# Kernel optimization log

Measured on AMD Instinct MI355X. Metric: run time of the kernel, lower is better.

The kernel has to match this reference:

```python
import jax, jax.numpy as jnp
import numpy as np

IN_DIM = 512
E = 512            # embed_dim
DI = 1024          # d_inner = expand * embed_dim
S = 16             # d_state
DC = 4             # d_conv
DT_RANK = 32       # ceil(embed_dim / 16)
NL = 2             # n_layers
N_SLICES = 8000
CHUNK = 500        # hard-coded batch_size in forward


def setup_inputs() -> dict:
    key = jax.random.key(0)
    ks = jax.random.split(key, 16)
    s = 0.02
    inp = {
        "slice_features": jax.random.normal(ks[0], (N_SLICES, IN_DIM), dtype=jnp.float32),
        "ip_w": jax.random.normal(ks[1], (E, IN_DIM), dtype=jnp.float32) * s,
        "ip_b": jnp.zeros((E,), jnp.float32),
        "in_ln_g": jnp.ones((E,), jnp.float32),
        "in_ln_b": jnp.zeros((E,), jnp.float32),
        "m_in_w": jax.random.normal(ks[2], (NL, 2 * DI, E), dtype=jnp.float32) * s,
        "m_conv_w": jax.random.normal(ks[3], (NL, DI, DC), dtype=jnp.float32) * s,
        "m_conv_b": jnp.zeros((NL, DI), jnp.float32),
        "m_xproj_w": jax.random.normal(ks[4], (NL, DT_RANK + 2 * S, DI), dtype=jnp.float32) * s,
        "m_dt_w": jax.random.normal(ks[5], (NL, DI, DT_RANK), dtype=jnp.float32) * s,
        "m_dt_b": jax.random.normal(ks[6], (NL, DI), dtype=jnp.float32) * 0.1,
        "m_Alog": jnp.log(jnp.tile(jnp.arange(1, S + 1, dtype=jnp.float32), (NL, DI, 1))),
        "m_D": jnp.ones((NL, DI), jnp.float32),
        "m_out_w": jax.random.normal(ks[7], (NL, E, DI), dtype=jnp.float32) * s,
        "ln_g": jnp.ones((NL, E), jnp.float32),
        "ln_b": jnp.zeros((NL, E), jnp.float32),
        "op_w": jax.random.normal(ks[8], (E, E), dtype=jnp.float32) * s,
        "op_b": jnp.zeros((E,), jnp.float32),
    }
    return inp


def _layer_norm(x, g, b):
    mu = jnp.mean(x, axis=-1, keepdims=True)
    var = jnp.mean(jnp.square(x - mu), axis=-1, keepdims=True)
    return (x - mu) * jax.lax.rsqrt(var + 1e-5) * g + b


def _mamba(h, in_w, conv_w, conv_b, xproj_w, dt_w, dt_b, Alog, Dp, out_w):
    # h: (Nc, L, E) -> (Nc, L, E)
    Nc, L, _ = h.shape
    xz = jnp.einsum('nle,de->nld', h, in_w)          # (Nc, L, 2*DI)
    x, z = jnp.split(xz, 2, axis=-1)
    # causal depthwise conv1d along L
    k = jnp.transpose(conv_w)[:, None, :]            # (DC, 1, DI) WIO grouped
    x = jax.lax.conv_general_dilated(
        x, k, window_strides=(1,), padding=[(DC - 1, 0)],
        dimension_numbers=('NWC', 'WIO', 'NWC'), feature_group_count=DI) + conv_b
    x = jax.nn.silu(x)
    x_dbl = jnp.einsum('nld,rd->nlr', x, xproj_w)    # (Nc, L, DT_RANK + 2S)
    dt = jax.nn.softplus(jnp.einsum('nlr,dr->nld', x_dbl[..., :DT_RANK], dt_w) + dt_b)
    B = x_dbl[..., DT_RANK:DT_RANK + S]
    C = x_dbl[..., DT_RANK + S:]
    A = -jnp.exp(Alog)                               # (DI, S)

    def step(hs, inp):
        dt_t, B_t, C_t, x_t = inp                    # (Nc,DI),(Nc,S),(Nc,S),(Nc,DI)
        dA = jnp.exp(dt_t[..., None] * A)            # (Nc, DI, S)
        hs = dA * hs + (dt_t * x_t)[..., None] * B_t[:, None, :]
        y = jnp.einsum('nds,ns->nd', hs, C_t)
        return hs, y

    xs = (jnp.swapaxes(dt, 0, 1), jnp.swapaxes(B, 0, 1),
          jnp.swapaxes(C, 0, 1), jnp.swapaxes(x, 0, 1))
    h0 = jnp.zeros((Nc, DI, S), dt.dtype)
    _, ys = jax.lax.scan(step, h0, xs)               # ys: (L, Nc, DI)
    y = jnp.swapaxes(ys, 0, 1) + x * Dp
    y = y * jax.nn.silu(z)
    return jnp.einsum('nld,ed->nle', y, out_w)


def reference(slice_features, ip_w, ip_b, in_ln_g, in_ln_b, m_in_w, m_conv_w, m_conv_b,
              m_xproj_w, m_dt_w, m_dt_b, m_Alog, m_D, m_out_w, ln_g, ln_b, op_w, op_b):
    h = slice_features @ ip_w.T + ip_b               # (N, E)
    h = _layer_norm(h, in_ln_g, in_ln_b)             # dropout: eval no-op
    h = h.reshape(N_SLICES // CHUNK, CHUNK, E)       # chunks of 500, batched
    for l in range(NL):
        res = h
        h = _mamba(h, m_in_w[l], m_conv_w[l], m_conv_b[l], m_xproj_w[l],
                   m_dt_w[l], m_dt_b[l], m_Alog[l], m_D[l], m_out_w[l])
        h = _layer_norm(h + res, ln_g[l], ln_b[l])
    h = h.reshape(N_SLICES, E)
    return h @ op_w.T + op_b
```

## Files before the change

kernel.cpp:

```cpp
#include <hip/hip_runtime.h>
#include <hip/hip_bf16.h>
#include <math.h>

#define NSL 8000
#define MPAD 8064
#define EDIM 512
#define DI_ 1024
#define SDIM 16
#define NLAY 2
#define CHK 500
#define PSEG 10
#define LSEG 50

typedef __bf16 bf16_t;
typedef bf16_t bf16x8 __attribute__((ext_vector_type(8)));
typedef bf16_t bf16x4 __attribute__((ext_vector_type(4)));
typedef float  f32x4  __attribute__((ext_vector_type(4)));

#define GL2LDS(g, l) __builtin_amdgcn_global_load_lds( \
    (const __attribute__((address_space(1))) void*)(g), \
    (__attribute__((address_space(3))) void*)(l), 16, 0, 0)

template<int EPI>
__global__ __launch_bounds__(256)
void gemm_mfma(const bf16_t* __restrict__ Ah, const bf16_t* __restrict__ Al,
               const bf16_t* __restrict__ Wh, const bf16_t* __restrict__ Wl,
               const float* __restrict__ bias, float* __restrict__ C,
               float* __restrict__ C2, int M, int N, int K)
{
    __shared__ bf16_t sm[4 * 128 * 64];
    const int tid = threadIdx.x;
    const int w   = tid >> 6;
    const int l   = tid & 63;
    const int m0  = blockIdx.y * 128;
    const int n0  = blockIdx.x * 128;

    const bf16_t* gb0 = Ah + (size_t)m0 * K;
    const bf16_t* gb1 = Al + (size_t)m0 * K;
    const bf16_t* gb2 = Wh + (size_t)n0 * K;
    const bf16_t* gb3 = Wl + (size_t)n0 * K;

    const int srow = l >> 3;
    const int scol = ((l & 7) ^ (l >> 3)) * 8;

    const int wm = (w >> 1) * 64;
    const int wn = (w & 1) * 64;
    const int lr = l & 15;
    const int lk = (l >> 4) * 8;
    const int csw = (l & 7) << 3;

    f32x4 acc[4][4];
    #pragma unroll
    for (int i = 0; i < 4; ++i)
        #pragma unroll
        for (int j = 0; j < 4; ++j) acc[i][j] = (f32x4){0.f,0.f,0.f,0.f};

    for (int kt = 0; kt < K; kt += 64) {
        #pragma unroll
        for (int i = 0; i < 16; ++i) {
            const int mat = i >> 2;
            const int lc  = ((i & 3) << 2) | w;
            const bf16_t* gsrc;
            if      (mat == 0) gsrc = gb0;
            else if (mat == 1) gsrc = gb1;
            else if (mat == 2) gsrc = gb2;
            else               gsrc = gb3;
            const bf16_t* gp = gsrc + (size_t)(lc * 8 + srow) * K + kt + scol;
            bf16_t* lp = sm + mat * 8192 + lc * 512;
            GL2LDS(gp, lp);
        }
        __syncthreads();
        #pragma unroll
        for (int ks = 0; ks < 2; ++ks) {
            bf16x8 ah[4], al[4], wh[4], wl[4];
            const int koff = (ks * 32 + lk) ^ csw;
            #pragma unroll
            for (int f = 0; f < 4; ++f) {
                const int ar = wm + f * 16 + lr;
                const int wr = wn + f * 16 + lr;
                ah[f] = *(const bf16x8*)(sm + 0 * 8192 + ar * 64 + koff);
                al[f] = *(const bf16x8*)(sm + 1 * 8192 + ar * 64 + koff);
                wh[f] = *(const bf16x8*)(sm + 2 * 8192 + wr * 64 + koff);
                wl[f] = *(const bf16x8*)(sm + 3 * 8192 + wr * 64 + koff);
            }
            #pragma unroll
            for (int fi = 0; fi < 4; ++fi)
                #pragma unroll
                for (int fj = 0; fj < 4; ++fj) {
                    acc[fi][fj] = __builtin_amdgcn_mfma_f32_16x16x32_bf16(ah[fi], wh[fj], acc[fi][fj], 0, 0, 0);
                    acc[fi][fj] = __builtin_amdgcn_mfma_f32_16x16x32_bf16(ah[fi], wl[fj], acc[fi][fj], 0, 0, 0);
                    acc[fi][fj] = __builtin_amdgcn_mfma_f32_16x16x32_bf16(al[fi], wh[fj], acc[fi][fj], 0, 0, 0);
                }
        }
        __syncthreads();
    }
    const int r4 = (l >> 4) * 4;
    #pragma unroll
    for (int fj = 0; fj < 4; ++fj) {
        const int col = n0 + wn + fj * 16 + lr;
        if (EPI == 3 && col >= 1056) continue;
        const float bv = (EPI == 1) ? bias[col]
                       : (EPI == 3 ? (col < 1024 ? bias[col] : 0.f) : 0.f);
        #pragma unroll
        for (int fi = 0; fi < 4; ++fi) {
            const int rowb = m0 + wm + fi * 16 + r4;
            #pragma unroll
            for (int r = 0; r < 4; ++r) {
                const int row = rowb + r;
                if (row >= M) continue;
                float v = acc[fi][fj][r] + bv;
                if (EPI == 3) {
                    if (col < 1024) {
                        v = fmaxf(v, 0.f) + log1pf(__expf(-fabsf(v)));
                        C[(size_t)row * 1024 + col] = v;
                    } else {
                        C2[(size_t)row * 32 + (col - 1024)] = v;
                    }
                } else {
                    C[(size_t)row * N + col] = v;
                }
            }
        }
    }
}

__global__ __launch_bounds__(256)
void compose_dtw(const float* __restrict__ dtw,
                 const float* __restrict__ xp,
                 bf16_t* __restrict__ wh, bf16_t* __restrict__ wl)
{
    const int d0 = blockIdx.x * 4;
    const int t  = threadIdx.x;
    float acc[4][4] = {{0.f}};
    for (int r = 0; r < 32; ++r) {
        float xv[4];
        #pragma unroll
        for (int cc = 0; cc < 4; ++cc) xv[cc] = xp[r * 1024 + t + cc * 256];
        #pragma unroll
        for (int dd = 0; dd < 4; ++dd) {
            float wv = dtw[(d0 + dd) * 32 + r];
            #pragma unroll
            for (int cc = 0; cc < 4; ++cc) acc[dd][cc] = fmaf(wv, xv[cc], acc[dd][cc]);
        }
    }
    #pragma unroll
    for (int dd = 0; dd < 4; ++dd)
        #pragma unroll
        for (int cc = 0; cc < 4; ++cc) {
            float v = acc[dd][cc];
            bf16_t hb = (bf16_t)v;
            size_t o = (size_t)(d0 + dd) * 1024 + t + cc * 256;
            wh[o] = hb;
            wl[o] = (bf16_t)(v - (float)hb);
        }
}

__global__ __launch_bounds__(256)
void ln_kernel(const float* __restrict__ in, const float* __restrict__ res,
               const float* __restrict__ g, const float* __restrict__ b,
               float* __restrict__ out, bf16_t* __restrict__ oh, bf16_t* __restrict__ ol)
{
    const int lane = threadIdx.x & 63;
    const int wv = threadIdx.x >> 6;
    const int row = blockIdx.x * 4 + wv;
    const size_t base = (size_t)row * EDIM + lane * 8;
    float x[8];
    float4 v0 = *(const float4*)(in + base);
    float4 v1 = *(const float4*)(in + base + 4);
    x[0]=v0.x; x[1]=v0.y; x[2]=v0.z; x[3]=v0.w;
    x[4]=v1.x; x[5]=v1.y; x[6]=v1.z; x[7]=v1.w;
    if (res) {
        float4 r0 = *(const float4*)(res + base);
        float4 r1 = *(const float4*)(res + base + 4);
        x[0]+=r0.x; x[1]+=r0.y; x[2]+=r0.z; x[3]+=r0.w;
        x[4]+=r1.x; x[5]+=r1.y; x[6]+=r1.z; x[7]+=r1.w;
    }
    float s = 0.f, sq = 0.f;
    #pragma unroll
    for (int j = 0; j < 8; ++j) { s += x[j]; sq += x[j]*x[j]; }
    #pragma unroll
    for (int off = 32; off; off >>= 1) {
        s  += __shfl_xor(s, off);
        sq += __shfl_xor(sq, off);
    }
    float mu = s * (1.f/EDIM);
    float var = sq * (1.f/EDIM) - mu*mu;
    float rs = rsqrtf(var + 1e-5f);
    const int col = lane * 8;
    float o[8];
    bf16x8 vh, vl;
    #pragma unroll
    for (int j = 0; j < 8; ++j) {
        o[j] = (x[j] - mu) * rs * g[col+j] + b[col+j];
        bf16_t hb = (bf16_t)o[j];
        vh[j] = hb;
        vl[j] = (bf16_t)(o[j] - (float)hb);
    }
    *(float4*)(out + base)     = make_float4(o[0],o[1],o[2],o[3]);
    *(float4*)(out + base + 4) = make_float4(o[4],o[5],o[6],o[7]);
    *(bf16x8*)(oh + base) = vh;
    *(bf16x8*)(ol + base) = vl;
}

__global__ __launch_bounds__(256)
void conv_silu_k(const float* __restrict__ xz, const float* __restrict__ w,
                 const float* __restrict__ b, bf16_t* __restrict__ xch,
                 bf16_t* __restrict__ xcl)
{
    const int d  = blockIdx.x * 256 + threadIdx.x;
    const int lc = blockIdx.y;
    const int n  = blockIdx.z;
    const int l0 = lc * 100;
    const float w0 = w[d*4+0], w1 = w[d*4+1], w2 = w[d*4+2], w3 = w[d*4+3];
    const float bb = b[d];
    const float* xp = xz + (size_t)n * CHK * 2048 + d;
    float x0 = (l0-3) >= 0 ? xp[(size_t)(l0-3)*2048] : 0.f;
    float x1 = (l0-2) >= 0 ? xp[(size_t)(l0-2)*2048] : 0.f;
    float x2 = (l0-1) >= 0 ? xp[(size_t)(l0-1)*2048] : 0.f;
    const size_t ob = ((size_t)n*CHK + l0) * DI_ + d;
    for (int l = 0; l < 100; ++l) {
        float x3 = xp[(size_t)(l0+l)*2048];
        float v = fmaf(w3,x3, fmaf(w2,x2, fmaf(w1,x1, fmaf(w0,x0, bb))));
        float sv = v / (1.f + __expf(-v));
        bf16_t hv = (bf16_t)sv;
        xch[ob + (size_t)l*DI_] = hv;
        xcl[ob + (size_t)l*DI_] = (bf16_t)(sv - (float)hv);
        x0 = x1; x1 = x2; x2 = x3;
    }
}

__global__ __launch_bounds__(256)
void sc_part(const float* __restrict__ dt, const bf16_t* __restrict__ xch,
             const bf16_t* __restrict__ xcl, const float* __restrict__ bc,
             const float* __restrict__ Alog,
             float* __restrict__ pA, float* __restrict__ loc)
{
    __shared__ float Bs[LSEG][SDIM];
    const int d  = blockIdx.x * 256 + threadIdx.x;
    const int n  = blockIdx.y;
    const int sg = blockIdx.z;
    const int t0 = sg * LSEG;
    const size_t rb = (size_t)n*CHK + t0;
    for (int idx = threadIdx.x; idx < LSEG*SDIM; idx += 256) {
        int t = idx >> 4, s = idx & 15;
        Bs[t][s] = bc[(rb + t)*32 + s];
    }
    __syncthreads();
    float A[SDIM], p[SDIM], lcl[SDIM];
    #pragma unroll
    for (int s = 0; s < SDIM; ++s) {
        A[s] = -__expf(Alog[d*SDIM + s]); p[s] = 1.f; lcl[s] = 0.f;
    }
    for (int t = 0; t < LSEG; ++t) {
        float dtv = dt[(rb+t)*DI_ + d];
        float xv  = (float)xch[(rb+t)*DI_ + d] + (float)xcl[(rb+t)*DI_ + d];
        float dx = dtv * xv;
        #pragma unroll
        for (int s = 0; s < SDIM; ++s) {
            float dA = __expf(dtv * A[s]);
            p[s] *= dA;
            lcl[s] = fmaf(dA, lcl[s], dx * Bs[t][s]);
        }
    }
    const size_t ob = ((size_t)(n*PSEG + sg) << 14) + d*16;
    #pragma unroll
    for (int s = 0; s < SDIM; s += 4) {
        *(float4*)(pA  + ob + s) = make_float4(p[s],p[s+1],p[s+2],p[s+3]);
        *(float4*)(loc + ob + s) = make_float4(lcl[s],lcl[s+1],lcl[s+2],lcl[s+3]);
    }
}

__global__ __launch_bounds__(256)
void sc_comb(const float* __restrict__ pA, float* __restrict__ hio)
{
    const int gI = blockIdx.x * 256 + threadIdx.x;
    const int n = gI >> 14;
    const int r = gI & 16383;
    float h = 0.f;
    #pragma unroll
    for (int sg = 0; sg < PSEG; ++sg) {
        size_t idx = ((size_t)(n*PSEG + sg) << 14) + r;
        float pa = pA[idx];
        float lo = hio[idx];
        hio[idx] = h;
        h = fmaf(pa, h, lo);
    }
}

__global__ __launch_bounds__(256)
void sc_fin(const float* __restrict__ dt, const bf16_t* __restrict__ xch,
            const bf16_t* __restrict__ xcl, const float* __restrict__ xz,
            const float* __restrict__ bc, const float* __restrict__ Alog,
            const float* __restrict__ Dp, const float* __restrict__ hin,
            bf16_t* __restrict__ yh, bf16_t* __restrict__ yl)
{
    __shared__ float BCs[LSEG][32];
    const int d  = blockIdx.x * 256 + threadIdx.x;
    const int n  = blockIdx.y;
    const int sg = blockIdx.z;
    const int t0 = sg * LSEG;
    const size_t rb = (size_t)n*CHK + t0;
    for (int idx = threadIdx.x; idx < LSEG*32; idx += 256) {
        int t = idx >> 5, s = idx & 31;
        BCs[t][s] = bc[(rb + t)*32 + s];
    }
    __syncthreads();
    float A[SDIM], h[SDIM];
    #pragma unroll
    for (int s = 0; s < SDIM; ++s) A[s] = -__expf(Alog[d*SDIM + s]);
    const size_t hb = ((size_t)(n*PSEG + sg) << 14) + d*16;
    #pragma unroll
    for (int s = 0; s < SDIM; ++s) h[s] = hin[hb + s];
    const float Dv = Dp[d];
    for (int t = 0; t < LSEG; ++t) {
        const size_t p = rb + t;
        float dtv = dt[p*DI_ + d];
        float xv  = (float)xch[p*DI_ + d] + (float)xcl[p*DI_ + d];
        float zv  = xz[p*2048 + DI_ + d];
        float dx = dtv * xv;
        float accv = 0.f;
        #pragma unroll
        for (int s = 0; s < SDIM; ++s) {
            float dA = __expf(dtv * A[s]);
            h[s] = fmaf(dA, h[s], dx * BCs[t][s]);
            accv = fmaf(h[s], BCs[t][16+s], accv);
        }
        float yv = fmaf(xv, Dv, accv);
        float sz = zv / (1.f + __expf(-zv));
        float outv = yv * sz;
        bf16_t oh = (bf16_t)outv;
        yh[p*DI_ + d] = oh;
        yl[p*DI_ + d] = (bf16_t)(outv - (float)oh);
    }
}

__global__ __launch_bounds__(256)
void convert_split(const float* __restrict__ src, bf16_t* __restrict__ hi,
                   bf16_t* __restrict__ lo, long n, long valid)
{
    long i = ((long)blockIdx.x * 256 + threadIdx.x) * 4;
    if (i >= n) return;
    float4 v = make_float4(0.f,0.f,0.f,0.f);
    if (i < valid) v = *(const float4*)(src + i);
    float a[4] = {v.x, v.y, v.z, v.w};
    bf16x4 vh, vl;
    #pragma unroll
    for (int j = 0; j < 4; ++j) {
        bf16_t hb = (bf16_t)a[j];
        vh[j] = hb;
        vl[j] = (bf16_t)(a[j] - (float)hb);
    }
    *(bf16x4*)(hi + i) = vh;
    *(bf16x4*)(lo + i) = vl;
}

extern "C" void kernel_launch(void* const* d_in, const int* in_sizes, int n_in,
                              void* d_out, int out_size, void* d_ws, size_t ws_size,
                              hipStream_t stream) {
    (void)in_sizes; (void)n_in; (void)out_size; (void)ws_size;
    const float* sf       = (const float*)d_in[0];
    const float* ip_w     = (const float*)d_in[1];
    const float* ip_b     = (const float*)d_in[2];
    const float* ilng     = (const float*)d_in[3];
    const float* ilnb     = (const float*)d_in[4];
    const float* m_in_w   = (const float*)d_in[5];
    const float* m_conv_w = (const float*)d_in[6];
    const float* m_conv_b = (const float*)d_in[7];
    const float* m_xproj_w= (const float*)d_in[8];
    const float* m_dt_w   = (const float*)d_in[9];
    const float* m_dt_b   = (const float*)d_in[10];
    const float* m_Alog   = (const float*)d_in[11];
    const float* m_D      = (const float*)d_in[12];
    const float* m_out_w  = (const float*)d_in[13];
    const float* ln_g     = (const float*)d_in[14];
    const float* ln_b     = (const float*)d_in[15];
    const float* op_w     = (const float*)d_in[16];
    const float* op_b     = (const float*)d_in[17];
    float* outp = (float*)d_out;

    float* t0   = (float*)d_ws;
    float* h    = t0   + 4096000;
    float* xzb  = h    + 4096000;
    float* dtb  = xzb  + 16384000;
    float* bcb  = dtb  + 8192000;
    float* pAb  = bcb  + 256000;
    float* locb = pAb  + 2621440;
    bf16_t* hh  = (bf16_t*)(locb + 2621440);
    bf16_t* hl  = hh  + 4128768;
    bf16_t* xch = hl  + 4128768;
    bf16_t* xcl = xch + 8257536;
    bf16_t* yh  = xcl + 8257536;
    bf16_t* yl  = yh  + 8257536;
    bf16_t* sfh = yh;
    bf16_t* sfl = yl;
    bf16_t* wiph = yl + 8257536;
    bf16_t* wipl = wiph + 262144;
    bf16_t* winh = wipl + 262144;
    bf16_t* winl = winh + 2097152;
    bf16_t* wouth= winl + 2097152;
    bf16_t* woutl= wouth + 1048576;
    bf16_t* woph = woutl + 1048576;
    bf16_t* wopl = woph + 262144;
    bf16_t* wcmbh= wopl + 262144;
    bf16_t* wcmbl= wcmbh + 1179648;

    dim3 blk(256);
    convert_split<<<256,  blk, 0, stream>>>(ip_w,    wiph, wipl, 262144,  262144);
    convert_split<<<2048, blk, 0, stream>>>(m_in_w,  winh, winl, 2097152, 2097152);
    convert_split<<<1024, blk, 0, stream>>>(m_out_w, wouth,woutl,1048576, 1048576);
    convert_split<<<256,  blk, 0, stream>>>(op_w,    woph, wopl, 262144,  262144);
    convert_split<<<4032, blk, 0, stream>>>(sf,      sfh,  sfl,  4128768, 4096000);

    gemm_mfma<1><<<dim3(4,63), blk, 0, stream>>>(sfh, sfl, wiph, wipl, ip_b, t0, nullptr, NSL, EDIM, 512);
    ln_kernel<<<2000, blk, 0, stream>>>(t0, nullptr, ilng, ilnb, h, hh, hl);

    for (int l = 0; l < NLAY; ++l) {
        const float* xp_l  = m_xproj_w + (size_t)l * 64 * 1024;
        gemm_mfma<0><<<dim3(16,63), blk, 0, stream>>>(hh, hl, winh + (size_t)l*1048576, winl + (size_t)l*1048576,
                                                      nullptr, xzb, nullptr, NSL, 2048, EDIM);
        conv_silu_k<<<dim3(4,5,16), blk, 0, stream>>>(xzb, m_conv_w + (size_t)l*DI_*4, m_conv_b + (size_t)l*DI_, xch, xcl);
        compose_dtw<<<256, blk, 0, stream>>>(m_dt_w + (size_t)l*DI_*32, xp_l, wcmbh, wcmbl);
        convert_split<<<32, blk, 0, stream>>>(xp_l + 32*1024, wcmbh + 1048576, wcmbl + 1048576, 32768, 32768);
        gemm_mfma<3><<<dim3(9,63), blk, 0, stream>>>(xch, xcl, wcmbh, wcmbl, m_dt_b + (size_t)l*DI_,
                                                     dtb, bcb, NSL, 1152, 1024);
        sc_part<<<dim3(4,16,PSEG), blk, 0, stream>>>(dtb, xch, xcl, bcb, m_Alog + (size_t)l*DI_*SDIM, pAb, locb);
        sc_comb<<<1024, blk, 0, stream>>>(pAb, locb);
        sc_fin<<<dim3(4,16,PSEG), blk, 0, stream>>>(dtb, xch, xcl, xzb, bcb, m_Alog + (size_t)l*DI_*SDIM,
                                                    m_D + (size_t)l*DI_, locb, yh, yl);
        gemm_mfma<0><<<dim3(4,63), blk, 0, stream>>>(yh, yl, wouth + (size_t)l*524288, woutl + (size_t)l*524288,
                                                     nullptr, t0, nullptr, NSL, EDIM, DI_);
        ln_kernel<<<2000, blk, 0, stream>>>(t0, h, ln_g + (size_t)l*EDIM, ln_b + (size_t)l*EDIM, h, hh, hl);
    }
    gemm_mfma<1><<<dim3(4,63), blk, 0, stream>>>(hh, hl, woph, wopl, op_b, outp, nullptr, NSL, EDIM, 512);
}
```

Measured before the change: 953.6 us.

## Load GEMM A fragments directly from global and template N-tile width

The split-bf16 GEMM no longer stages the A operand (hi/lo) in LDS. Each lane reads its A fragments straight from global memory into registers, and only the W operand goes through LDS. The N tile width becomes a template parameter, so the N=512 GEMMs run with 64-wide tiles and twice as many blocks, and launch bounds request 4 waves per SIMD for occupancy. The aim is to cut LDS traffic and footprint and to fill more CUs on the small GEMMs. The cost is uncoalesced, unprefetched 16-byte global loads for A issued inside the MFMA loop, plus more redundant A reads across N tiles.

```diff
diff --git a/kernel.cpp b/kernel.cpp
--- a/kernel.cpp
+++ b/kernel.cpp
@@ -21,72 +21,77 @@
     (const __attribute__((address_space(1))) void*)(g), \
     (__attribute__((address_space(3))) void*)(l), 16, 0, 0)
 
-template<int EPI>
-__global__ __launch_bounds__(256)
+template<int EPI, int NF>
+__global__ __launch_bounds__(256, 4)
 void gemm_mfma(const bf16_t* __restrict__ Ah, const bf16_t* __restrict__ Al,
                const bf16_t* __restrict__ Wh, const bf16_t* __restrict__ Wl,
                const float* __restrict__ bias, float* __restrict__ C,
                float* __restrict__ C2, int M, int N, int K)
 {
-    __shared__ bf16_t sm[4 * 128 * 64];
+    constexpr int BN = NF * 32;
+    __shared__ bf16_t sm[2 * BN * 64];
     const int tid = threadIdx.x;
     const int w   = tid >> 6;
     const int l   = tid & 63;
     const int m0  = blockIdx.y * 128;
-    const int n0  = blockIdx.x * 128;
-
-    const bf16_t* gb0 = Ah + (size_t)m0 * K;
-    const bf16_t* gb1 = Al + (size_t)m0 * K;
-    const bf16_t* gb2 = Wh + (size_t)n0 * K;
-    const bf16_t* gb3 = Wl + (size_t)n0 * K;
+    const int n0  = blockIdx.x * BN;
+
+    const bf16_t* gw0 = Wh + (size_t)n0 * K;
+    const bf16_t* gw1 = Wl + (size_t)n0 * K;
 
     const int srow = l >> 3;
     const int scol = ((l & 7) ^ (l >> 3)) * 8;
 
     const int wm = (w >> 1) * 64;
-    const int wn = (w & 1) * 64;
+    const int wn = (w & 1) * (NF * 16);
     const int lr = l & 15;
     const int lk = (l >> 4) * 8;
     const int csw = (l & 7) << 3;
 
-    f32x4 acc[4][4];
+    const bf16_t* aph[4];
+    const bf16_t* apl[4];
+    #pragma unroll
+    for (int f = 0; f < 4; ++f) {
+        const int r = m0 + wm + f * 16 + lr;
+        aph[f] = Ah + (size_t)r * K + lk;
+        apl[f] = Al + (size_t)r * K + lk;
+    }
+
+    f32x4 acc[4][NF];
     #pragma unroll
     for (int i = 0; i < 4; ++i)
         #pragma unroll
-        for (int j = 0; j < 4; ++j) acc[i][j] = (f32x4){0.f,0.f,0.f,0.f};
+        for (int j = 0; j < NF; ++j) acc[i][j] = (f32x4){0.f,0.f,0.f,0.f};
 
     for (int kt = 0; kt < K; kt += 64) {
         #pragma unroll
-        for (int i = 0; i < 16; ++i) {
-            const int mat = i >> 2;
-            const int lc  = ((i & 3) << 2) | w;
-            const bf16_t* gsrc;
-            if      (mat == 0) gsrc = gb0;
-            else if (mat == 1) gsrc = gb1;
-            else if (mat == 2) gsrc = gb2;
-            else               gsrc = gb3;
-            const bf16_t* gp = gsrc + (size_t)(lc * 8 + srow) * K + kt + scol;
-            bf16_t* lp = sm + mat * 8192 + lc * 512;
-            GL2LDS(gp, lp);
+        for (int i = 0; i < BN / 32; ++i) {
+            const int lc = (i << 2) | w;
+            const size_t go = (size_t)(lc * 8 + srow) * K + kt + scol;
+            GL2LDS(gw0 + go, sm + lc * 512);
+            GL2LDS(gw1 + go, sm + BN * 64 + lc * 512);
         }
         __syncthreads();
         #pragma unroll
         for (int ks = 0; ks < 2; ++ks) {
-            bf16x8 ah[4], al[4], wh[4], wl[4];
+            bf16x8 ah[4], al[4], wh[NF], wl[NF];
+            const int ko = kt + ks * 32;
+            #pragma unroll
+            for (int f = 0; f < 4; ++f) {
+                ah[f] = *(const bf16x8*)(aph[f] + ko);
+                al[f] = *(const bf16x8*)(apl[f] + ko);
+            }
             const int koff = (ks * 32 + lk) ^ csw;
             #pragma unroll
-            for (int f = 0; f < 4; ++f) {
-                const int ar = wm + f * 16 + lr;
+            for (int f = 0; f < NF; ++f) {
                 const int wr = wn + f * 16 + lr;
-                ah[f] = *(const bf16x8*)(sm + 0 * 8192 + ar * 64 + koff);
-                al[f] = *(const bf16x8*)(sm + 1 * 8192 + ar * 64 + koff);
-                wh[f] = *(const bf16x8*)(sm + 2 * 8192 + wr * 64 + koff);
-                wl[f] = *(const bf16x8*)(sm + 3 * 8192 + wr * 64 + koff);
+                wh[f] = *(const bf16x8*)(sm + wr * 64 + koff);
+                wl[f] = *(const bf16x8*)(sm + BN * 64 + wr * 64 + koff);
             }
             #pragma unroll
             for (int fi = 0; fi < 4; ++fi)
                 #pragma unroll
-                for (int fj = 0; fj < 4; ++fj) {
+                for (int fj = 0; fj < NF; ++fj) {
                     acc[fi][fj] = __builtin_amdgcn_mfma_f32_16x16x32_bf16(ah[fi], wh[fj], acc[fi][fj], 0, 0, 0);
                     acc[fi][fj] = __builtin_amdgcn_mfma_f32_16x16x32_bf16(ah[fi], wl[fj], acc[fi][fj], 0, 0, 0);
                     acc[fi][fj] = __builtin_amdgcn_mfma_f32_16x16x32_bf16(al[fi], wh[fj], acc[fi][fj], 0, 0, 0);
@@ -96,7 +101,7 @@
     }
     const int r4 = (l >> 4) * 4;
     #pragma unroll
-    for (int fj = 0; fj < 4; ++fj) {
+    for (int fj = 0; fj < NF; ++fj) {
         const int col = n0 + wn + fj * 16 + lr;
         if (EPI == 3 && col >= 1056) continue;
         const float bv = (EPI == 1) ? bias[col]
@@ -411,25 +416,25 @@
     convert_split<<<256,  blk, 0, stream>>>(op_w,    woph, wopl, 262144,  262144);
     convert_split<<<4032, blk, 0, stream>>>(sf,      sfh,  sfl,  4128768, 4096000);
 
-    gemm_mfma<1><<<dim3(4,63), blk, 0, stream>>>(sfh, sfl, wiph, wipl, ip_b, t0, nullptr, NSL, EDIM, 512);
+    gemm_mfma<1,2><<<dim3(8,63), blk, 0, stream>>>(sfh, sfl, wiph, wipl, ip_b, t0, nullptr, NSL, EDIM, 512);
     ln_kernel<<<2000, blk, 0, stream>>>(t0, nullptr, ilng, ilnb, h, hh, hl);
 
     for (int l = 0; l < NLAY; ++l) {
         const float* xp_l  = m_xproj_w + (size_t)l * 64 * 1024;
-        gemm_mfma<0><<<dim3(16,63), blk, 0, stream>>>(hh, hl, winh + (size_t)l*1048576, winl + (size_t)l*1048576,
-                                                      nullptr, xzb, nullptr, NSL, 2048, EDIM);
+        gemm_mfma<0,4><<<dim3(16,63), blk, 0, stream>>>(hh, hl, winh + (size_t)l*1048576, winl + (size_t)l*1048576,
+                                                        nullptr, xzb, nullptr, NSL, 2048, EDIM);
         conv_silu_k<<<dim3(4,5,16), blk, 0, stream>>>(xzb, m_conv_w + (size_t)l*DI_*4, m_conv_b + (size_t)l*DI_, xch, xcl);
         compose_dtw<<<256, blk, 0, stream>>>(m_dt_w + (size_t)l*DI_*32, xp_l, wcmbh, wcmbl);
         convert_split<<<32, blk, 0, stream>>>(xp_l + 32*1024, wcmbh + 1048576, wcmbl + 1048576, 32768, 32768);
-        gemm_mfma<3><<<dim3(9,63), blk, 0, stream>>>(xch, xcl, wcmbh, wcmbl, m_dt_b + (size_t)l*DI_,
-                                                     dtb, bcb, NSL, 1152, 1024);
+        gemm_mfma<3,4><<<dim3(9,63), blk, 0, stream>>>(xch, xcl, wcmbh, wcmbl, m_dt_b + (size_t)l*DI_,
+                                                       dtb, bcb, NSL, 1152, 1024);
         sc_part<<<dim3(4,16,PSEG), blk, 0, stream>>>(dtb, xch, xcl, bcb, m_Alog + (size_t)l*DI_*SDIM, pAb, locb);
         sc_comb<<<1024, blk, 0, stream>>>(pAb, locb);
         sc_fin<<<dim3(4,16,PSEG), blk, 0, stream>>>(dtb, xch, xcl, xzb, bcb, m_Alog + (size_t)l*DI_*SDIM,
                                                     m_D + (size_t)l*DI_, locb, yh, yl);
-        gemm_mfma<0><<<dim3(4,63), blk, 0, stream>>>(yh, yl, wouth + (size_t)l*524288, woutl + (size_t)l*524288,
-                                                     nullptr, t0, nullptr, NSL, EDIM, DI_);
+        gemm_mfma<0,2><<<dim3(8,63), blk, 0, stream>>>(yh, yl, wouth + (size_t)l*524288, woutl + (size_t)l*524288,
+                                                       nullptr, t0, nullptr, NSL, EDIM, DI_);
         ln_kernel<<<2000, blk, 0, stream>>>(t0, h, ln_g + (size_t)l*EDIM, ln_b + (size_t)l*EDIM, h, hh, hl);
     }
-    gemm_mfma<1><<<dim3(4,63), blk, 0, stream>>>(hh, hl, woph, wopl, op_b, outp, nullptr, NSL, EDIM, 512);
-}
+    gemm_mfma<1,2><<<dim3(8,63), blk, 0, stream>>>(hh, hl, woph, wopl, op_b, outp, nullptr, NSL, EDIM, 512);
+}
```

Measured after the change: 1.407 ms. +47.5%, slower.

## Halve GEMM LDS tile by packing hi/lo bf16 halves into one K-32 tile

Applied to the files above, without the earlier changes.

The split-bf16 GEMM now stages a K-step of 32 per iteration, with the hi and lo halves of each operand packed side by side in one 64-column LDS row. This halves shared memory per block from 64KB to 32KB. It also adds launch_bounds min-blocks 4 so more blocks can reside per CU to hide latency. In exchange there are twice as many loop iterations and barriers per K, and the register cap may force spills.

```diff
diff --git a/kernel.cpp b/kernel.cpp
--- a/kernel.cpp
+++ b/kernel.cpp
@@ -22,32 +22,41 @@
     (__attribute__((address_space(3))) void*)(l), 16, 0, 0)
 
 template<int EPI>
-__global__ __launch_bounds__(256)
+__global__ __launch_bounds__(256, 4)
 void gemm_mfma(const bf16_t* __restrict__ Ah, const bf16_t* __restrict__ Al,
                const bf16_t* __restrict__ Wh, const bf16_t* __restrict__ Wl,
                const float* __restrict__ bias, float* __restrict__ C,
                float* __restrict__ C2, int M, int N, int K)
 {
-    __shared__ bf16_t sm[4 * 128 * 64];
+    __shared__ bf16_t sm[2 * 128 * 64];
     const int tid = threadIdx.x;
     const int w   = tid >> 6;
     const int l   = tid & 63;
     const int m0  = blockIdx.y * 128;
     const int n0  = blockIdx.x * 128;
 
-    const bf16_t* gb0 = Ah + (size_t)m0 * K;
-    const bf16_t* gb1 = Al + (size_t)m0 * K;
-    const bf16_t* gb2 = Wh + (size_t)n0 * K;
-    const bf16_t* gb3 = Wl + (size_t)n0 * K;
-
-    const int srow = l >> 3;
-    const int scol = ((l & 7) ^ (l >> 3)) * 8;
-
-    const int wm = (w >> 1) * 64;
-    const int wn = (w & 1) * 64;
-    const int lr = l & 15;
-    const int lk = (l >> 4) * 8;
+    const int srow  = l >> 3;
+    const int sslot = (l & 7) ^ srow;
+    const int sc    = sslot * 8;
+    const bf16_t* asrc[4];
+    const bf16_t* wsrc[4];
+    #pragma unroll
+    for (int i = 0; i < 4; ++i) {
+        const int lc  = (i << 2) | w;
+        const int row = lc * 8 + srow;
+        asrc[i] = (sc < 32) ? Ah + (size_t)(m0 + row) * K + sc
+                            : Al + (size_t)(m0 + row) * K + (sc - 32);
+        wsrc[i] = (sc < 32) ? Wh + (size_t)(n0 + row) * K + sc
+                            : Wl + (size_t)(n0 + row) * K + (sc - 32);
+    }
+
+    const int wm  = (w >> 1) * 64;
+    const int wn  = (w & 1) * 64;
+    const int lr  = l & 15;
+    const int lk  = (l >> 4) * 8;
     const int csw = (l & 7) << 3;
+    const int cHi = lk ^ csw;
+    const int cLo = (32 + lk) ^ csw;
 
     f32x4 acc[4][4];
     #pragma unroll
@@ -55,43 +64,32 @@
         #pragma unroll
         for (int j = 0; j < 4; ++j) acc[i][j] = (f32x4){0.f,0.f,0.f,0.f};
 
-    for (int kt = 0; kt < K; kt += 64) {
-        #pragma unroll
-        for (int i = 0; i < 16; ++i) {
-            const int mat = i >> 2;
-            const int lc  = ((i & 3) << 2) | w;
-            const bf16_t* gsrc;
-            if      (mat == 0) gsrc = gb0;
-            else if (mat == 1) gsrc = gb1;
-            else if (mat == 2) gsrc = gb2;
-            else               gsrc = gb3;
-            const bf16_t* gp = gsrc + (size_t)(lc * 8 + srow) * K + kt + scol;
-            bf16_t* lp = sm + mat * 8192 + lc * 512;
-            GL2LDS(gp, lp);
+    for (int kt = 0; kt < K; kt += 32) {
+        #pragma unroll
+        for (int i = 0; i < 4; ++i) {
+            const int lc = (i << 2) | w;
+            GL2LDS(asrc[i] + kt, sm + lc * 512);
+            GL2LDS(wsrc[i] + kt, sm + 8192 + lc * 512);
         }
         __syncthreads();
-        #pragma unroll
-        for (int ks = 0; ks < 2; ++ks) {
-            bf16x8 ah[4], al[4], wh[4], wl[4];
-            const int koff = (ks * 32 + lk) ^ csw;
+        bf16x8 ah[4], al[4], wh[4], wl[4];
+        #pragma unroll
+        for (int f = 0; f < 4; ++f) {
+            const int ar = (wm + f * 16 + lr) * 64;
+            const int wr = (wn + f * 16 + lr) * 64;
+            ah[f] = *(const bf16x8*)(sm + ar + cHi);
+            al[f] = *(const bf16x8*)(sm + ar + cLo);
+            wh[f] = *(const bf16x8*)(sm + 8192 + wr + cHi);
+            wl[f] = *(const bf16x8*)(sm + 8192 + wr + cLo);
+        }
+        #pragma unroll
+        for (int fi = 0; fi < 4; ++fi)
             #pragma unroll
-            for (int f = 0; f < 4; ++f) {
-                const int ar = wm + f * 16 + lr;
-                const int wr = wn + f * 16 + lr;
-                ah[f] = *(const bf16x8*)(sm + 0 * 8192 + ar * 64 + koff);
-                al[f] = *(const bf16x8*)(sm + 1 * 8192 + ar * 64 + koff);
-                wh[f] = *(const bf16x8*)(sm + 2 * 8192 + wr * 64 + koff);
-                wl[f] = *(const bf16x8*)(sm + 3 * 8192 + wr * 64 + koff);
+            for (int fj = 0; fj < 4; ++fj) {
+                acc[fi][fj] = __builtin_amdgcn_mfma_f32_16x16x32_bf16(ah[fi], wh[fj], acc[fi][fj], 0, 0, 0);
+                acc[fi][fj] = __builtin_amdgcn_mfma_f32_16x16x32_bf16(ah[fi], wl[fj], acc[fi][fj], 0, 0, 0);
+                acc[fi][fj] = __builtin_amdgcn_mfma_f32_16x16x32_bf16(al[fi], wh[fj], acc[fi][fj], 0, 0, 0);
             }
-            #pragma unroll
-            for (int fi = 0; fi < 4; ++fi)
-                #pragma unroll
-                for (int fj = 0; fj < 4; ++fj) {
-                    acc[fi][fj] = __builtin_amdgcn_mfma_f32_16x16x32_bf16(ah[fi], wh[fj], acc[fi][fj], 0, 0, 0);
-                    acc[fi][fj] = __builtin_amdgcn_mfma_f32_16x16x32_bf16(ah[fi], wl[fj], acc[fi][fj], 0, 0, 0);
-                    acc[fi][fj] = __builtin_amdgcn_mfma_f32_16x16x32_bf16(al[fi], wh[fj], acc[fi][fj], 0, 0, 0);
-                }
-        }
         __syncthreads();
     }
     const int r4 = (l >> 4) * 4;
```

New measurement: 918.8 us. 1.04x faster.
